# Kernel optimization log

Hardware: AMD Instinct MI355X
Metric: run time of the kernel (lower is better)

Reference implementation:

```python
import jax, jax.numpy as jnp
import numpy as np

B = 65536   # batch (agent-timesteps)
NN = 16     # neighbors per agent
NO = 32     # obstacles per agent
SD = 4      # state_dim_per_agent
D_ROBOT = 0.3
D_OBST = 0.5
B_GAMMA = 0.01
B_EXPH = 1.0
A_MIN, A_MAX = -2.0, 2.0
PHI_MIN, PHI_MAX = -2.0, 2.0


def _mlp2(h, W1, b1, W2, b2):
    # DeepSet sub-network: activation between layers, linear last (matches
    # 'for layer in layers[:-1]: x = act(layer(x)); x = layers[-1](x)')
    return jax.nn.relu(h @ W1 + b1) @ W2 + b2


def setup_inputs() -> dict:
    key = jax.random.key(0)
    ks = jax.random.split(key, 24)
    own = jax.random.normal(ks[0], (B, SD), dtype=jnp.float32)
    # relative positions with |component| in [0.5, 2.0] so norms exceed D_* (barrier well-defined)
    npos = jax.random.uniform(ks[1], (B, NN, 2), minval=0.5, maxval=2.0) * jnp.sign(jax.random.normal(ks[2], (B, NN, 2)))
    nvel = 0.1 * jax.random.normal(ks[3], (B, NN, 2))
    neigh = jnp.concatenate([npos, nvel], axis=-1).reshape(B, 4 * NN)
    opos = (jax.random.uniform(ks[4], (B, NO, 2), minval=0.5, maxval=2.0) * jnp.sign(jax.random.normal(ks[5], (B, NO, 2)))).reshape(B, 2 * NO)
    x = jnp.concatenate([jnp.full((B, 1), float(NN), dtype=jnp.float32), own, neigh, opos], axis=1)
    noise = 0.05 * jax.random.normal(ks[6], (B, 2), dtype=jnp.float32)  # the 0.05*N(0,1) action noise, made deterministic

    def lin(k, i, o):
        return 0.1 * jax.random.normal(k, (i, o), dtype=jnp.float32)

    return {
        'x': x, 'noise': noise,
        # neighbor DeepSet: phi 4->64->16, rho 16->64->8
        'pnW1': lin(ks[7], 4, 64),  'pnb1': jnp.zeros((64,), jnp.float32),
        'pnW2': lin(ks[8], 64, 16), 'pnb2': jnp.zeros((16,), jnp.float32),
        'rnW1': lin(ks[9], 16, 64), 'rnb1': jnp.zeros((64,), jnp.float32),
        'rnW2': lin(ks[10], 64, 8), 'rnb2': jnp.zeros((8,), jnp.float32),
        # obstacle DeepSet: phi 2->64->16, rho 16->64->8
        'poW1': lin(ks[11], 2, 64),  'pob1': jnp.zeros((64,), jnp.float32),
        'poW2': lin(ks[12], 64, 16), 'pob2': jnp.zeros((16,), jnp.float32),
        'roW1': lin(ks[13], 16, 64), 'rob1': jnp.zeros((64,), jnp.float32),
        'roW2': lin(ks[14], 64, 8),  'rob2': jnp.zeros((8,), jnp.float32),
        # psi: 18 -> 64 -> 64 -> 2
        'psW1': lin(ks[15], 18, 64), 'psb1': jnp.zeros((64,), jnp.float32),
        'psW2': lin(ks[16], 64, 64), 'psb2': jnp.zeros((64,), jnp.float32),
        'psW3': lin(ks[17], 64, 2),  'psb3': jnp.zeros((2,), jnp.float32),
    }


def reference(x, noise,
              pnW1, pnb1, pnW2, pnb2, rnW1, rnb1, rnW2, rnb2,
              poW1, pob1, poW2, pob2, roW1, rob1, roW2, rob2,
              psW1, psb1, psW2, psb2, psW3, psb3):
    b = x.shape[0]
    neigh = x[:, 5:5 + 4 * NN].reshape(b, NN, 4)   # per-neighbor relative state
    obst = x[:, 5 + 4 * NN:].reshape(b, NO, 2)      # per-obstacle relative pos

    # 'empty' (learned) action: DeepSets + psi MLP
    rho_n = _mlp2(_mlp2(neigh, pnW1, pnb1, pnW2, pnb2).sum(axis=1), rnW1, rnb1, rnW2, rnb2)
    rho_o = _mlp2(_mlp2(obst, poW1, pob1, poW2, pob2).sum(axis=1), roW1, rob1, roW2, rob2)
    g = x[:, 1:3]
    h = jnp.concatenate([rho_n, rho_o, g], axis=1)
    h = jax.nn.relu(h @ psW1 + psb1)
    h = jax.nn.relu(h @ psW2 + psb2)
    h = jnp.tanh(h @ psW3 + psb3)
    empty = (h + 1.0) / 2.0 * (PHI_MAX - PHI_MIN) + PHI_MIN

    # barrier terms, vectorized over all neighbors/obstacles at once:
    # A = b_gamma * P * ||P||^-1 * (||P|| - D)^(-b_exph), summed over edges
    def barrier_sum(P, D):
        nrm = jnp.linalg.norm(P, axis=-1, keepdims=True)   # [b, E, 1]
        H = nrm - D
        return (B_GAMMA * P / (nrm * H ** B_EXPH)).sum(axis=1)

    bar = barrier_sum(-neigh[..., :2], D_ROBOT) + barrier_sum(-obst, D_OBST)

    a = jnp.tanh(empty + bar + noise)
    return (a + 1.0) / 2.0 * (A_MAX - A_MIN) + A_MIN
```

## Files before the change

kernel.cpp:

```cpp
#include <hip/hip_runtime.h>

#define NN 16
#define NO 32
#define XCOLS 133

typedef _Float16 h8v __attribute__((ext_vector_type(8)));
typedef float f4v __attribute__((ext_vector_type(4)));
typedef unsigned ui4 __attribute__((ext_vector_type(4)));
typedef float f4u __attribute__((ext_vector_type(4), aligned(4)));

static __device__ __forceinline__ f4v MFMA(h8v a, h8v b, f4v c) {
    return __builtin_amdgcn_mfma_f32_16x16x32_f16(a, b, c, 0, 0, 0);
}
static __device__ __forceinline__ unsigned pkbits(float a, float b) {
    return __builtin_bit_cast(unsigned, __builtin_amdgcn_cvt_pkrtz(a, b));
}

__global__ void prep_frags(
    const float* __restrict__ pnW1, const float* __restrict__ pnW2,
    const float* __restrict__ rnW1, const float* __restrict__ rnW2,
    const float* __restrict__ poW1, const float* __restrict__ poW2,
    const float* __restrict__ roW1, const float* __restrict__ roW2,
    const float* __restrict__ psW1, const float* __restrict__ psW2,
    const float* __restrict__ psW3, unsigned* __restrict__ ws)
{
    const float* Ws[11] = {pnW1,pnW2,rnW1,rnW2,poW1,poW2,roW1,roW2,psW1,psW2,psW3};
    const int Kr[11]   = {4,64,16,64,2,64,16,64,18,64,64};
    const int Nr[11]   = {64,16,64,8,64,16,64,8,64,64,2};
    const int nkc[11]  = {1,2,1,2,1,2,1,2,1,2,2};
    const int nnt[11]  = {4,1,4,1,4,1,4,1,4,4,1};
    const int base[11] = {0,1024,1536,2560,3072,4096,4608,5632,6144,7168,9216};

    const int gid = blockIdx.x * 256 + threadIdx.x;
    int start = 0;
    #pragma unroll
    for (int a2 = 0; a2 < 11; ++a2) {
        const int n = nkc[a2] * nnt[a2] * 256;
        if (gid >= start && gid < start + n) {
            const int i = gid - start;
            const float* Wm = Ws[a2];
            const int K = Kr[a2], N = Nr[a2], nt_n = nnt[a2];
            const int d = i & 3, lane = (i >> 2) & 63, t = i >> 8;
            const int nt = t % nt_n, kc = t / nt_n;
            const int k = kc * 32 + 8 * (lane >> 4) + 2 * d;
            const int col = nt * 16 + (lane & 15);
            const float v0 = (k     < K && col < N) ? Wm[(k    ) * N + col] : 0.f;
            const float v1 = (k + 1 < K && col < N) ? Wm[(k + 1) * N + col] : 0.f;
            ws[base[a2] + i] = pkbits(v0, v1);
        }
        start += n;
    }
}

__global__ __launch_bounds__(64, 8) void barrier_net_kernel(
    const float* __restrict__ x, const float* __restrict__ noise,
    const float* __restrict__ pnb1, const float* __restrict__ pnb2,
    const float* __restrict__ rnb1, const float* __restrict__ rnb2,
    const float* __restrict__ pob1, const float* __restrict__ pob2,
    const float* __restrict__ rob1, const float* __restrict__ rob2,
    const float* __restrict__ psb1, const float* __restrict__ psb2,
    const float* __restrict__ psb3,
    const unsigned* __restrict__ wsu, float* __restrict__ out)
{
    __shared__ _Float16 W[3136];

    const int l = threadIdx.x;
    const int r = l & 15;
    const int g = l >> 4;
    const int eb = blockIdx.x * 16;

    float* barf = (float*)(W + 3072);
    const h8v* FB = (const h8v*)wsu;

    {
        unsigned* z = (unsigned*)(W + 2048);
        #pragma unroll
        for (int i = 0; i < 8; ++i) z[l + 64 * i] = 0u;
    }

    const size_t xrow = (size_t)(eb + r) * XCOLS;

    {
        float bq0 = 0.f, bq1 = 0.f;
        const float* pxn = x + xrow + 5;
        #pragma unroll
        for (int jj = 0; jj < 4; ++jj) {
            const int j = 4 * g + jj;
            const float v0 = pxn[4*j], v1 = pxn[4*j + 1];
            const float nrm = sqrtf(v0*v0 + v1*v1);
            const float cc = 0.01f * __builtin_amdgcn_rcpf(nrm * (nrm - 0.3f));
            bq0 -= cc * v0; bq1 -= cc * v1;
        }
        const float* pxo = x + xrow + 69;
        #pragma unroll
        for (int jj = 0; jj < 8; ++jj) {
            const int j = 8 * g + jj;
            const float v0 = pxo[2*j], v1 = pxo[2*j + 1];
            const float nrm = sqrtf(v0*v0 + v1*v1);
            const float cc = 0.01f * __builtin_amdgcn_rcpf(nrm * (nrm - 0.5f));
            bq0 -= cc * v0; bq1 -= cc * v1;
        }
        bq0 += __shfl_xor(bq0, 16); bq0 += __shfl_xor(bq0, 32);
        bq1 += __shfl_xor(bq1, 16); bq1 += __shfl_xor(bq1, 32);
        if (g == 0) { barf[2*r] = bq0; barf[2*r + 1] = bq1; }
    }

    {
        const h8v B0 = FB[0*64 + l], B1 = FB[1*64 + l];
        const h8v B2 = FB[2*64 + l], B3 = FB[3*64 + l];
        const f4v c0 = {pnb1[r], pnb1[r], pnb1[r], pnb1[r]};
        const f4v c1 = {pnb1[16+r], pnb1[16+r], pnb1[16+r], pnb1[16+r]};
        const f4v c2 = {pnb1[32+r], pnb1[32+r], pnb1[32+r], pnb1[32+r]};
        const f4v c3 = {pnb1[48+r], pnb1[48+r], pnb1[48+r], pnb1[48+r]};
        f4v s0 = {0,0,0,0}, s1 = {0,0,0,0}, s2 = {0,0,0,0}, s3 = {0,0,0,0};
        const float* px = x + xrow + 5;
        #pragma unroll 4
        for (int j = 0; j < NN; ++j) {
            const f4u v = *(const f4u*)(px + 4*j);
            ui4 au = {pkbits(v[0], v[1]), pkbits(v[2], v[3]), 0u, 0u};
            const h8v a = __builtin_bit_cast(h8v, au);
            const f4v d0 = MFMA(a, B0, c0);
            const f4v d1 = MFMA(a, B1, c1);
            const f4v d2 = MFMA(a, B2, c2);
            const f4v d3 = MFMA(a, B3, c3);
            #pragma unroll
            for (int q = 0; q < 4; ++q) {
                s0[q] += fmaxf(d0[q], 0.f); s1[q] += fmaxf(d1[q], 0.f);
                s2[q] += fmaxf(d2[q], 0.f); s3[q] += fmaxf(d3[q], 0.f);
            }
        }
        #pragma unroll
        for (int q = 0; q < 4; ++q) {
            const int e = 4 * g + q;
            const int m = (e & 7) << 3;
            W[e*64 + (( 0 + r) ^ m)] = (_Float16)s0[q];
            W[e*64 + ((16 + r) ^ m)] = (_Float16)s1[q];
            W[e*64 + ((32 + r) ^ m)] = (_Float16)s2[q];
            W[e*64 + ((48 + r) ^ m)] = (_Float16)s3[q];
        }
    }

    {
        const h8v B0 = FB[768 + 0*64 + l], B1 = FB[768 + 1*64 + l];
        const h8v B2 = FB[768 + 2*64 + l], B3 = FB[768 + 3*64 + l];
        const f4v c0 = {pob1[r], pob1[r], pob1[r], pob1[r]};
        const f4v c1 = {pob1[16+r], pob1[16+r], pob1[16+r], pob1[16+r]};
        const f4v c2 = {pob1[32+r], pob1[32+r], pob1[32+r], pob1[32+r]};
        const f4v c3 = {pob1[48+r], pob1[48+r], pob1[48+r], pob1[48+r]};
        f4v s0 = {0,0,0,0}, s1 = {0,0,0,0}, s2 = {0,0,0,0}, s3 = {0,0,0,0};
        const float* px = x + xrow + 69;
        #pragma unroll 2
        for (int t = 0; t < 16; ++t) {
            const f4u v = *(const f4u*)(px + 4*t);
            ui4 au0 = {pkbits(v[0], v[1]), 0u, 0u, 0u};
            ui4 au1 = {pkbits(v[2], v[3]), 0u, 0u, 0u};
            const h8v a0 = __builtin_bit_cast(h8v, au0);
            const h8v a1 = __builtin_bit_cast(h8v, au1);
            const f4v d0 = MFMA(a0, B0, c0); const f4v e0 = MFMA(a1, B0, c0);
            const f4v d1 = MFMA(a0, B1, c1); const f4v e1 = MFMA(a1, B1, c1);
            const f4v d2 = MFMA(a0, B2, c2); const f4v e2 = MFMA(a1, B2, c2);
            const f4v d3 = MFMA(a0, B3, c3); const f4v e3 = MFMA(a1, B3, c3);
            #pragma unroll
            for (int q = 0; q < 4; ++q) {
                s0[q] += fmaxf(d0[q], 0.f) + fmaxf(e0[q], 0.f);
                s1[q] += fmaxf(d1[q], 0.f) + fmaxf(e1[q], 0.f);
                s2[q] += fmaxf(d2[q], 0.f) + fmaxf(e2[q], 0.f);
                s3[q] += fmaxf(d3[q], 0.f) + fmaxf(e3[q], 0.f);
            }
        }
        #pragma unroll
        for (int q = 0; q < 4; ++q) {
            const int e = 4 * g + q;
            const int m = (e & 7) << 3;
            W[1024 + e*64 + (( 0 + r) ^ m)] = (_Float16)s0[q];
            W[1024 + e*64 + ((16 + r) ^ m)] = (_Float16)s1[q];
            W[1024 + e*64 + ((32 + r) ^ m)] = (_Float16)s2[q];
            W[1024 + e*64 + ((48 + r) ^ m)] = (_Float16)s3[q];
        }
    }

    {
        h8v a0 = *(const h8v*)&W[r*64 + (( 0 + 8*g) ^ ((r&7)<<3))];
        h8v a1 = *(const h8v*)&W[r*64 + ((32 + 8*g) ^ ((r&7)<<3))];
        h8v b0 = FB[256 + 0*64 + l];
        h8v b1 = FB[256 + 1*64 + l];
        const float bb = 16.f * pnb2[r];
        f4v c = {bb, bb, bb, bb};
        f4v d = MFMA(a1, b1, MFMA(a0, b0, c));
        #pragma unroll
        for (int q = 0; q < 4; ++q) {
            const int row = 4 * g + q;
            W[2048 + row*32 + (r ^ ((row&3)<<3))] = (_Float16)d[q];
        }
    }
    {
        h8v a = *(const h8v*)&W[2048 + r*32 + ((8*g) ^ ((r&3)<<3))];
        #pragma unroll
        for (int nt = 0; nt < 4; ++nt) {
            h8v b = FB[384 + nt*64 + l];
            const float bb = rnb1[16*nt + r];
            f4v c = {bb, bb, bb, bb};
            f4v d = MFMA(a, b, c);
            #pragma unroll
            for (int q = 0; q < 4; ++q) {
                const int row = 4 * g + q;
                W[row*64 + ((16*nt + r) ^ ((row&7)<<3))] = (_Float16)fmaxf(d[q], 0.f);
            }
        }
    }
    {
        h8v a0 = *(const h8v*)&W[r*64 + (( 0 + 8*g) ^ ((r&7)<<3))];
        h8v a1 = *(const h8v*)&W[r*64 + ((32 + 8*g) ^ ((r&7)<<3))];
        h8v b0 = FB[640 + 0*64 + l];
        h8v b1 = FB[640 + 1*64 + l];
        const float bb = (r < 8) ? rnb2[r & 7] : 0.f;
        f4v c = {bb, bb, bb, bb};
        f4v d = MFMA(a1, b1, MFMA(a0, b0, c));
        if (r < 8) {
            #pragma unroll
            for (int q = 0; q < 4; ++q) {
                const int row = 4 * g + q;
                W[2560 + row*32 + (r ^ ((row&3)<<3))] = (_Float16)d[q];
            }
        }
    }
    {
        h8v a0 = *(const h8v*)&W[1024 + r*64 + (( 0 + 8*g) ^ ((r&7)<<3))];
        h8v a1 = *(const h8v*)&W[1024 + r*64 + ((32 + 8*g) ^ ((r&7)<<3))];
        h8v b0 = FB[1024 + 0*64 + l];
        h8v b1 = FB[1024 + 1*64 + l];
        const float bb = 32.f * pob2[r];
        f4v c = {bb, bb, bb, bb};
        f4v d = MFMA(a1, b1, MFMA(a0, b0, c));
        #pragma unroll
        for (int q = 0; q < 4; ++q) {
            const int row = 4 * g + q;
            W[2048 + row*32 + (r ^ ((row&3)<<3))] = (_Float16)d[q];
        }
    }
    {
        h8v a = *(const h8v*)&W[2048 + r*32 + ((8*g) ^ ((r&3)<<3))];
        #pragma unroll
        for (int nt = 0; nt < 4; ++nt) {
            h8v b = FB[1152 + nt*64 + l];
            const float bb = rob1[16*nt + r];
            f4v c = {bb, bb, bb, bb};
            f4v d = MFMA(a, b, c);
            #pragma unroll
            for (int q = 0; q < 4; ++q) {
                const int row = 4 * g + q;
                W[row*64 + ((16*nt + r) ^ ((row&7)<<3))] = (_Float16)fmaxf(d[q], 0.f);
            }
        }
    }
    {
        h8v a0 = *(const h8v*)&W[r*64 + (( 0 + 8*g) ^ ((r&7)<<3))];
        h8v a1 = *(const h8v*)&W[r*64 + ((32 + 8*g) ^ ((r&7)<<3))];
        h8v b0 = FB[1408 + 0*64 + l];
        h8v b1 = FB[1408 + 1*64 + l];
        const float bb = (r < 8) ? rob2[r & 7] : 0.f;
        f4v c = {bb, bb, bb, bb};
        f4v d = MFMA(a1, b1, MFMA(a0, b0, c));
        if (r < 8) {
            #pragma unroll
            for (int q = 0; q < 4; ++q) {
                const int row = 4 * g + q;
                W[2560 + row*32 + ((8 + r) ^ ((row&3)<<3))] = (_Float16)d[q];
            }
        }
    }
    if (g == 0) {
        const float gx = x[xrow + 1];
        const float gy = x[xrow + 2];
        W[2560 + r*32 + (16 ^ ((r&3)<<3))] = (_Float16)gx;
        W[2560 + r*32 + (17 ^ ((r&3)<<3))] = (_Float16)gy;
    }
    {
        h8v a = *(const h8v*)&W[2560 + r*32 + ((8*g) ^ ((r&3)<<3))];
        #pragma unroll
        for (int nt = 0; nt < 4; ++nt) {
            h8v b = FB[1536 + nt*64 + l];
            const float bb = psb1[16*nt + r];
            f4v c = {bb, bb, bb, bb};
            f4v d = MFMA(a, b, c);
            #pragma unroll
            for (int q = 0; q < 4; ++q) {
                const int row = 4 * g + q;
                W[1024 + row*64 + ((16*nt + r) ^ ((row&7)<<3))] = (_Float16)fmaxf(d[q], 0.f);
            }
        }
    }
    {
        h8v a0 = *(const h8v*)&W[1024 + r*64 + (( 0 + 8*g) ^ ((r&7)<<3))];
        h8v a1 = *(const h8v*)&W[1024 + r*64 + ((32 + 8*g) ^ ((r&7)<<3))];
        #pragma unroll
        for (int nt = 0; nt < 4; ++nt) {
            h8v b0 = FB[1792 + (0*4 + nt)*64 + l];
            h8v b1 = FB[1792 + (1*4 + nt)*64 + l];
            const float bb = psb2[16*nt + r];
            f4v c = {bb, bb, bb, bb};
            f4v d = MFMA(a1, b1, MFMA(a0, b0, c));
            #pragma unroll
            for (int q = 0; q < 4; ++q) {
                const int row = 4 * g + q;
                W[row*64 + ((16*nt + r) ^ ((row&7)<<3))] = (_Float16)fmaxf(d[q], 0.f);
            }
        }
    }
    f4v dOut;
    {
        h8v a0 = *(const h8v*)&W[r*64 + (( 0 + 8*g) ^ ((r&7)<<3))];
        h8v a1 = *(const h8v*)&W[r*64 + ((32 + 8*g) ^ ((r&7)<<3))];
        h8v b0 = FB[2304 + 0*64 + l];
        h8v b1 = FB[2304 + 1*64 + l];
        const float bb = (r < 2) ? psb3[r & 1] : 0.f;
        f4v c = {bb, bb, bb, bb};
        dOut = MFMA(a1, b1, MFMA(a0, b0, c));
    }
    if (r < 2) {
        #pragma unroll
        for (int q = 0; q < 4; ++q) {
            const int e = 4 * g + q;
            const float o = dOut[q];
            const float bar = barf[e*2 + r];
            const float nz = noise[2 * (size_t)(eb + e) + r];
            const float av = tanhf(2.f * tanhf(o) + bar + nz);
            out[2 * (size_t)(eb + e) + r] = 2.f * av;
        }
    }
}

extern "C" void kernel_launch(void* const* d_in, const int* in_sizes, int n_in,
                              void* d_out, int out_size, void* d_ws, size_t ws_size,
                              hipStream_t stream) {
    const float* x    = (const float*)d_in[0];
    const float* nz   = (const float*)d_in[1];
    const float* pnW1 = (const float*)d_in[2];
    const float* pnb1 = (const float*)d_in[3];
    const float* pnW2 = (const float*)d_in[4];
    const float* pnb2 = (const float*)d_in[5];
    const float* rnW1 = (const float*)d_in[6];
    const float* rnb1 = (const float*)d_in[7];
    const float* rnW2 = (const float*)d_in[8];
    const float* rnb2 = (const float*)d_in[9];
    const float* poW1 = (const float*)d_in[10];
    const float* pob1 = (const float*)d_in[11];
    const float* poW2 = (const float*)d_in[12];
    const float* pob2 = (const float*)d_in[13];
    const float* roW1 = (const float*)d_in[14];
    const float* rob1 = (const float*)d_in[15];
    const float* roW2 = (const float*)d_in[16];
    const float* rob2 = (const float*)d_in[17];
    const float* psW1 = (const float*)d_in[18];
    const float* psb1 = (const float*)d_in[19];
    const float* psW2 = (const float*)d_in[20];
    const float* psb2 = (const float*)d_in[21];
    const float* psW3 = (const float*)d_in[22];
    const float* psb3 = (const float*)d_in[23];

    unsigned* ws = (unsigned*)d_ws;
    hipLaunchKernelGGL(prep_frags, dim3(38), dim3(256), 0, stream,
        pnW1, pnW2, rnW1, rnW2, poW1, poW2, roW1, roW2, psW1, psW2, psW3, ws);

    const int b = in_sizes[0] / XCOLS;
    hipLaunchKernelGGL(barrier_net_kernel, dim3(b / 16), dim3(64), 0, stream,
        x, nz, pnb1, pnb2, rnb1, rnb2, pob1, pob2, rob1, rob2,
        psb1, psb2, psb3, ws, (float*)d_out);
}
```

Before: 45.44 us.

## Fuse neighbor and obstacle DeepSet stages and pack four waves per block

```diff
diff --git a/kernel.cpp b/kernel.cpp
--- a/kernel.cpp
+++ b/kernel.cpp
@@ -52,7 +52,7 @@
     }
 }
 
-__global__ __launch_bounds__(64, 8) void barrier_net_kernel(
+__global__ __launch_bounds__(256, 4) void barrier_net_kernel(
     const float* __restrict__ x, const float* __restrict__ noise,
     const float* __restrict__ pnb1, const float* __restrict__ pnb2,
     const float* __restrict__ rnb1, const float* __restrict__ rnb2,
@@ -62,23 +62,88 @@
     const float* __restrict__ psb3,
     const unsigned* __restrict__ wsu, float* __restrict__ out)
 {
-    __shared__ _Float16 W[3136];
-
-    const int l = threadIdx.x;
+    __shared__ _Float16 smem[4][3648];
+
+    const int tid = threadIdx.x;
+    const int l = tid & 63;
+    const int w = tid >> 6;
     const int r = l & 15;
     const int g = l >> 4;
-    const int eb = blockIdx.x * 16;
-
-    float* barf = (float*)(W + 3072);
+    const int eb = blockIdx.x * 64 + w * 16;
+
+    _Float16* W = &smem[w][0];
+    float* barf = (float*)(W + 3584);
     const h8v* FB = (const h8v*)wsu;
 
     {
         unsigned* z = (unsigned*)(W + 2048);
         #pragma unroll
-        for (int i = 0; i < 8; ++i) z[l + 64 * i] = 0u;
+        for (int i = 0; i < 12; ++i) z[l + 64 * i] = 0u;
     }
 
     const size_t xrow = (size_t)(eb + r) * XCOLS;
+    const int sw8 = (r & 7) << 3;
+    const int sw4 = (r & 3) << 3;
+
+    {
+        const h8v BN0 = FB[0*64 + l], BN1 = FB[1*64 + l];
+        const h8v BN2 = FB[2*64 + l], BN3 = FB[3*64 + l];
+        const h8v BO0 = FB[768 + 0*64 + l], BO1 = FB[768 + 1*64 + l];
+        const h8v BO2 = FB[768 + 2*64 + l], BO3 = FB[768 + 3*64 + l];
+        const f4v cN0 = {pnb1[r], pnb1[r], pnb1[r], pnb1[r]};
+        const f4v cN1 = {pnb1[16+r], pnb1[16+r], pnb1[16+r], pnb1[16+r]};
+        const f4v cN2 = {pnb1[32+r], pnb1[32+r], pnb1[32+r], pnb1[32+r]};
+        const f4v cN3 = {pnb1[48+r], pnb1[48+r], pnb1[48+r], pnb1[48+r]};
+        const f4v cO0 = {pob1[r], pob1[r], pob1[r], pob1[r]};
+        const f4v cO1 = {pob1[16+r], pob1[16+r], pob1[16+r], pob1[16+r]};
+        const f4v cO2 = {pob1[32+r], pob1[32+r], pob1[32+r], pob1[32+r]};
+        const f4v cO3 = {pob1[48+r], pob1[48+r], pob1[48+r], pob1[48+r]};
+        f4v sN0 = {0,0,0,0}, sN1 = {0,0,0,0}, sN2 = {0,0,0,0}, sN3 = {0,0,0,0};
+        f4v sO0 = {0,0,0,0}, sO1 = {0,0,0,0}, sO2 = {0,0,0,0}, sO3 = {0,0,0,0};
+        const float* pxn = x + xrow + 5;
+        const float* pxo = x + xrow + 69;
+        #pragma unroll 2
+        for (int t = 0; t < 16; ++t) {
+            const f4u vN = *(const f4u*)(pxn + 4*t);
+            const f4u vO = *(const f4u*)(pxo + 4*t);
+            ui4 auN = {pkbits(vN[0], vN[1]), pkbits(vN[2], vN[3]), 0u, 0u};
+            ui4 auO0 = {pkbits(vO[0], vO[1]), 0u, 0u, 0u};
+            ui4 auO1 = {pkbits(vO[2], vO[3]), 0u, 0u, 0u};
+            const h8v aN  = __builtin_bit_cast(h8v, auN);
+            const h8v aO0 = __builtin_bit_cast(h8v, auO0);
+            const h8v aO1 = __builtin_bit_cast(h8v, auO1);
+            const f4v dN0 = MFMA(aN, BN0, cN0);
+            const f4v dN1 = MFMA(aN, BN1, cN1);
+            const f4v dN2 = MFMA(aN, BN2, cN2);
+            const f4v dN3 = MFMA(aN, BN3, cN3);
+            const f4v dO0 = MFMA(aO0, BO0, cO0); const f4v eO0 = MFMA(aO1, BO0, cO0);
+            const f4v dO1 = MFMA(aO0, BO1, cO1); const f4v eO1 = MFMA(aO1, BO1, cO1);
+            const f4v dO2 = MFMA(aO0, BO2, cO2); const f4v eO2 = MFMA(aO1, BO2, cO2);
+            const f4v dO3 = MFMA(aO0, BO3, cO3); const f4v eO3 = MFMA(aO1, BO3, cO3);
+            #pragma unroll
+            for (int q = 0; q < 4; ++q) {
+                sN0[q] += fmaxf(dN0[q], 0.f); sN1[q] += fmaxf(dN1[q], 0.f);
+                sN2[q] += fmaxf(dN2[q], 0.f); sN3[q] += fmaxf(dN3[q], 0.f);
+                sO0[q] += fmaxf(dO0[q], 0.f) + fmaxf(eO0[q], 0.f);
+                sO1[q] += fmaxf(dO1[q], 0.f) + fmaxf(eO1[q], 0.f);
+                sO2[q] += fmaxf(dO2[q], 0.f) + fmaxf(eO2[q], 0.f);
+                sO3[q] += fmaxf(dO3[q], 0.f) + fmaxf(eO3[q], 0.f);
+            }
+        }
+        #pragma unroll
+        for (int q = 0; q < 4; ++q) {
+            const int e = 4 * g + q;
+            const int m = (e & 7) << 3;
+            W[e*64 + (( 0 + r) ^ m)] = (_Float16)sN0[q];
+            W[e*64 + ((16 + r) ^ m)] = (_Float16)sN1[q];
+            W[e*64 + ((32 + r) ^ m)] = (_Float16)sN2[q];
+            W[e*64 + ((48 + r) ^ m)] = (_Float16)sN3[q];
+            W[1024 + e*64 + (( 0 + r) ^ m)] = (_Float16)sO0[q];
+            W[1024 + e*64 + ((16 + r) ^ m)] = (_Float16)sO1[q];
+            W[1024 + e*64 + ((32 + r) ^ m)] = (_Float16)sO2[q];
+            W[1024 + e*64 + ((48 + r) ^ m)] = (_Float16)sO3[q];
+        }
+    }
 
     {
         float bq0 = 0.f, bq1 = 0.f;
@@ -106,177 +171,79 @@
     }
 
     {
-        const h8v B0 = FB[0*64 + l], B1 = FB[1*64 + l];
-        const h8v B2 = FB[2*64 + l], B3 = FB[3*64 + l];
-        const f4v c0 = {pnb1[r], pnb1[r], pnb1[r], pnb1[r]};
-        const f4v c1 = {pnb1[16+r], pnb1[16+r], pnb1[16+r], pnb1[16+r]};
-        const f4v c2 = {pnb1[32+r], pnb1[32+r], pnb1[32+r], pnb1[32+r]};
-        const f4v c3 = {pnb1[48+r], pnb1[48+r], pnb1[48+r], pnb1[48+r]};
-        f4v s0 = {0,0,0,0}, s1 = {0,0,0,0}, s2 = {0,0,0,0}, s3 = {0,0,0,0};
-        const float* px = x + xrow + 5;
-        #pragma unroll 4
-        for (int j = 0; j < NN; ++j) {
-            const f4u v = *(const f4u*)(px + 4*j);
-            ui4 au = {pkbits(v[0], v[1]), pkbits(v[2], v[3]), 0u, 0u};
-            const h8v a = __builtin_bit_cast(h8v, au);
-            const f4v d0 = MFMA(a, B0, c0);
-            const f4v d1 = MFMA(a, B1, c1);
-            const f4v d2 = MFMA(a, B2, c2);
-            const f4v d3 = MFMA(a, B3, c3);
-            #pragma unroll
-            for (int q = 0; q < 4; ++q) {
-                s0[q] += fmaxf(d0[q], 0.f); s1[q] += fmaxf(d1[q], 0.f);
-                s2[q] += fmaxf(d2[q], 0.f); s3[q] += fmaxf(d3[q], 0.f);
-            }
-        }
-        #pragma unroll
-        for (int q = 0; q < 4; ++q) {
-            const int e = 4 * g + q;
-            const int m = (e & 7) << 3;
-            W[e*64 + (( 0 + r) ^ m)] = (_Float16)s0[q];
-            W[e*64 + ((16 + r) ^ m)] = (_Float16)s1[q];
-            W[e*64 + ((32 + r) ^ m)] = (_Float16)s2[q];
-            W[e*64 + ((48 + r) ^ m)] = (_Float16)s3[q];
-        }
-    }
-
-    {
-        const h8v B0 = FB[768 + 0*64 + l], B1 = FB[768 + 1*64 + l];
-        const h8v B2 = FB[768 + 2*64 + l], B3 = FB[768 + 3*64 + l];
-        const f4v c0 = {pob1[r], pob1[r], pob1[r], pob1[r]};
-        const f4v c1 = {pob1[16+r], pob1[16+r], pob1[16+r], pob1[16+r]};
-        const f4v c2 = {pob1[32+r], pob1[32+r], pob1[32+r], pob1[32+r]};
-        const f4v c3 = {pob1[48+r], pob1[48+r], pob1[48+r], pob1[48+r]};
-        f4v s0 = {0,0,0,0}, s1 = {0,0,0,0}, s2 = {0,0,0,0}, s3 = {0,0,0,0};
-        const float* px = x + xrow + 69;
-        #pragma unroll 2
-        for (int t = 0; t < 16; ++t) {
-            const f4u v = *(const f4u*)(px + 4*t);
-            ui4 au0 = {pkbits(v[0], v[1]), 0u, 0u, 0u};
-            ui4 au1 = {pkbits(v[2], v[3]), 0u, 0u, 0u};
-            const h8v a0 = __builtin_bit_cast(h8v, au0);
-            const h8v a1 = __builtin_bit_cast(h8v, au1);
-            const f4v d0 = MFMA(a0, B0, c0); const f4v e0 = MFMA(a1, B0, c0);
-            const f4v d1 = MFMA(a0, B1, c1); const f4v e1 = MFMA(a1, B1, c1);
-            const f4v d2 = MFMA(a0, B2, c2); const f4v e2 = MFMA(a1, B2, c2);
-            const f4v d3 = MFMA(a0, B3, c3); const f4v e3 = MFMA(a1, B3, c3);
-            #pragma unroll
-            for (int q = 0; q < 4; ++q) {
-                s0[q] += fmaxf(d0[q], 0.f) + fmaxf(e0[q], 0.f);
-                s1[q] += fmaxf(d1[q], 0.f) + fmaxf(e1[q], 0.f);
-                s2[q] += fmaxf(d2[q], 0.f) + fmaxf(e2[q], 0.f);
-                s3[q] += fmaxf(d3[q], 0.f) + fmaxf(e3[q], 0.f);
-            }
-        }
-        #pragma unroll
-        for (int q = 0; q < 4; ++q) {
-            const int e = 4 * g + q;
-            const int m = (e & 7) << 3;
-            W[1024 + e*64 + (( 0 + r) ^ m)] = (_Float16)s0[q];
-            W[1024 + e*64 + ((16 + r) ^ m)] = (_Float16)s1[q];
-            W[1024 + e*64 + ((32 + r) ^ m)] = (_Float16)s2[q];
-            W[1024 + e*64 + ((48 + r) ^ m)] = (_Float16)s3[q];
-        }
-    }
-
-    {
-        h8v a0 = *(const h8v*)&W[r*64 + (( 0 + 8*g) ^ ((r&7)<<3))];
-        h8v a1 = *(const h8v*)&W[r*64 + ((32 + 8*g) ^ ((r&7)<<3))];
-        h8v b0 = FB[256 + 0*64 + l];
-        h8v b1 = FB[256 + 1*64 + l];
-        const float bb = 16.f * pnb2[r];
-        f4v c = {bb, bb, bb, bb};
-        f4v d = MFMA(a1, b1, MFMA(a0, b0, c));
+        h8v aN0 = *(const h8v*)&W[r*64 + (( 0 + 8*g) ^ sw8)];
+        h8v aN1 = *(const h8v*)&W[r*64 + ((32 + 8*g) ^ sw8)];
+        h8v aO0 = *(const h8v*)&W[1024 + r*64 + (( 0 + 8*g) ^ sw8)];
+        h8v aO1 = *(const h8v*)&W[1024 + r*64 + ((32 + 8*g) ^ sw8)];
+        h8v bN0 = FB[256 + 0*64 + l], bN1 = FB[256 + 1*64 + l];
+        h8v bO0 = FB[1024 + 0*64 + l], bO1 = FB[1024 + 1*64 + l];
+        const float bbN = 16.f * pnb2[r];
+        const float bbO = 32.f * pob2[r];
+        f4v cN = {bbN, bbN, bbN, bbN};
+        f4v cO = {bbO, bbO, bbO, bbO};
+        f4v dN = MFMA(aN1, bN1, MFMA(aN0, bN0, cN));
+        f4v dO = MFMA(aO1, bO1, MFMA(aO0, bO0, cO));
         #pragma unroll
         for (int q = 0; q < 4; ++q) {
             const int row = 4 * g + q;
-            W[2048 + row*32 + (r ^ ((row&3)<<3))] = (_Float16)d[q];
-        }
-    }
-    {
-        h8v a = *(const h8v*)&W[2048 + r*32 + ((8*g) ^ ((r&3)<<3))];
+            const int sm = (row & 3) << 3;
+            W[2048 + row*32 + (r ^ sm)] = (_Float16)dN[q];
+            W[2560 + row*32 + (r ^ sm)] = (_Float16)dO[q];
+        }
+    }
+    {
+        h8v aN = *(const h8v*)&W[2048 + r*32 + ((8*g) ^ sw4)];
+        h8v aO = *(const h8v*)&W[2560 + r*32 + ((8*g) ^ sw4)];
         #pragma unroll
         for (int nt = 0; nt < 4; ++nt) {
-            h8v b = FB[384 + nt*64 + l];
-            const float bb = rnb1[16*nt + r];
-            f4v c = {bb, bb, bb, bb};
-            f4v d = MFMA(a, b, c);
+            h8v bN = FB[384 + nt*64 + l];
+            h8v bO = FB[1152 + nt*64 + l];
+            const float bbN = rnb1[16*nt + r];
+            const float bbO = rob1[16*nt + r];
+            f4v cN = {bbN, bbN, bbN, bbN};
+            f4v cO = {bbO, bbO, bbO, bbO};
+            f4v dN = MFMA(aN, bN, cN);
+            f4v dO = MFMA(aO, bO, cO);
             #pragma unroll
             for (int q = 0; q < 4; ++q) {
                 const int row = 4 * g + q;
-                W[row*64 + ((16*nt + r) ^ ((row&7)<<3))] = (_Float16)fmaxf(d[q], 0.f);
-            }
-        }
-    }
-    {
-        h8v a0 = *(const h8v*)&W[r*64 + (( 0 + 8*g) ^ ((r&7)<<3))];
-        h8v a1 = *(const h8v*)&W[r*64 + ((32 + 8*g) ^ ((r&7)<<3))];
-        h8v b0 = FB[640 + 0*64 + l];
-        h8v b1 = FB[640 + 1*64 + l];
-        const float bb = (r < 8) ? rnb2[r & 7] : 0.f;
-        f4v c = {bb, bb, bb, bb};
-        f4v d = MFMA(a1, b1, MFMA(a0, b0, c));
+                const int sm = (row & 7) << 3;
+                W[row*64 + ((16*nt + r) ^ sm)] = (_Float16)fmaxf(dN[q], 0.f);
+                W[1024 + row*64 + ((16*nt + r) ^ sm)] = (_Float16)fmaxf(dO[q], 0.f);
+            }
+        }
+    }
+    {
+        h8v aN0 = *(const h8v*)&W[r*64 + (( 0 + 8*g) ^ sw8)];
+        h8v aN1 = *(const h8v*)&W[r*64 + ((32 + 8*g) ^ sw8)];
+        h8v aO0 = *(const h8v*)&W[1024 + r*64 + (( 0 + 8*g) ^ sw8)];
+        h8v aO1 = *(const h8v*)&W[1024 + r*64 + ((32 + 8*g) ^ sw8)];
+        h8v bN0 = FB[640 + 0*64 + l], bN1 = FB[640 + 1*64 + l];
+        h8v bO0 = FB[1408 + 0*64 + l], bO1 = FB[1408 + 1*64 + l];
+        const float bbN = (r < 8) ? rnb2[r & 7] : 0.f;
+        const float bbO = (r < 8) ? rob2[r & 7] : 0.f;
+        f4v cN = {bbN, bbN, bbN, bbN};
+        f4v cO = {bbO, bbO, bbO, bbO};
+        f4v dN = MFMA(aN1, bN1, MFMA(aN0, bN0, cN));
+        f4v dO = MFMA(aO1, bO1, MFMA(aO0, bO0, cO));
         if (r < 8) {
             #pragma unroll
             for (int q = 0; q < 4; ++q) {
                 const int row = 4 * g + q;
-                W[2560 + row*32 + (r ^ ((row&3)<<3))] = (_Float16)d[q];
-            }
-        }
-    }
-    {
-        h8v a0 = *(const h8v*)&W[1024 + r*64 + (( 0 + 8*g) ^ ((r&7)<<3))];
-        h8v a1 = *(const h8v*)&W[1024 + r*64 + ((32 + 8*g) ^ ((r&7)<<3))];
-        h8v b0 = FB[1024 + 0*64 + l];
-        h8v b1 = FB[1024 + 1*64 + l];
-        const float bb = 32.f * pob2[r];
-        f4v c = {bb, bb, bb, bb};
-        f4v d = MFMA(a1, b1, MFMA(a0, b0, c));
-        #pragma unroll
-        for (int q = 0; q < 4; ++q) {
-            const int row = 4 * g + q;
-            W[2048 + row*32 + (r ^ ((row&3)<<3))] = (_Float16)d[q];
-        }
-    }
-    {
-        h8v a = *(const h8v*)&W[2048 + r*32 + ((8*g) ^ ((r&3)<<3))];
-        #pragma unroll
-        for (int nt = 0; nt < 4; ++nt) {
-            h8v b = FB[1152 + nt*64 + l];
-            const float bb = rob1[16*nt + r];
-            f4v c = {bb, bb, bb, bb};
-            f4v d = MFMA(a, b, c);
-            #pragma unroll
-            for (int q = 0; q < 4; ++q) {
-                const int row = 4 * g + q;
-                W[row*64 + ((16*nt + r) ^ ((row&7)<<3))] = (_Float16)fmaxf(d[q], 0.f);
-            }
-        }
-    }
-    {
-        h8v a0 = *(const h8v*)&W[r*64 + (( 0 + 8*g) ^ ((r&7)<<3))];
-        h8v a1 = *(const h8v*)&W[r*64 + ((32 + 8*g) ^ ((r&7)<<3))];
-        h8v b0 = FB[1408 + 0*64 + l];
-        h8v b1 = FB[1408 + 1*64 + l];
-        const float bb = (r < 8) ? rob2[r & 7] : 0.f;
-        f4v c = {bb, bb, bb, bb};
-        f4v d = MFMA(a1, b1, MFMA(a0, b0, c));
-        if (r < 8) {
-            #pragma unroll
-            for (int q = 0; q < 4; ++q) {
-                const int row = 4 * g + q;
-                W[2560 + row*32 + ((8 + r) ^ ((row&3)<<3))] = (_Float16)d[q];
+                const int sm = (row & 3) << 3;
+                W[3072 + row*32 + (r ^ sm)] = (_Float16)dN[q];
+                W[3072 + row*32 + ((8 + r) ^ sm)] = (_Float16)dO[q];
             }
         }
     }
     if (g == 0) {
         const float gx = x[xrow + 1];
         const float gy = x[xrow + 2];
-        W[2560 + r*32 + (16 ^ ((r&3)<<3))] = (_Float16)gx;
-        W[2560 + r*32 + (17 ^ ((r&3)<<3))] = (_Float16)gy;
-    }
-    {
-        h8v a = *(const h8v*)&W[2560 + r*32 + ((8*g) ^ ((r&3)<<3))];
+        W[3072 + r*32 + (16 ^ sw4)] = (_Float16)gx;
+        W[3072 + r*32 + (17 ^ sw4)] = (_Float16)gy;
+    }
+    {
+        h8v a = *(const h8v*)&W[3072 + r*32 + ((8*g) ^ sw4)];
         #pragma unroll
         for (int nt = 0; nt < 4; ++nt) {
             h8v b = FB[1536 + nt*64 + l];
@@ -286,13 +253,13 @@
             #pragma unroll
             for (int q = 0; q < 4; ++q) {
                 const int row = 4 * g + q;
-                W[1024 + row*64 + ((16*nt + r) ^ ((row&7)<<3))] = (_Float16)fmaxf(d[q], 0.f);
-            }
-        }
-    }
-    {
-        h8v a0 = *(const h8v*)&W[1024 + r*64 + (( 0 + 8*g) ^ ((r&7)<<3))];
-        h8v a1 = *(const h8v*)&W[1024 + r*64 + ((32 + 8*g) ^ ((r&7)<<3))];
+                W[1024 + row*64 + ((16*nt + r) ^ ((row & 7) << 3))] = (_Float16)fmaxf(d[q], 0.f);
+            }
+        }
+    }
+    {
+        h8v a0 = *(const h8v*)&W[1024 + r*64 + (( 0 + 8*g) ^ sw8)];
+        h8v a1 = *(const h8v*)&W[1024 + r*64 + ((32 + 8*g) ^ sw8)];
         #pragma unroll
         for (int nt = 0; nt < 4; ++nt) {
             h8v b0 = FB[1792 + (0*4 + nt)*64 + l];
@@ -303,14 +270,14 @@
             #pragma unroll
             for (int q = 0; q < 4; ++q) {
                 const int row = 4 * g + q;
-                W[row*64 + ((16*nt + r) ^ ((row&7)<<3))] = (_Float16)fmaxf(d[q], 0.f);
+                W[row*64 + ((16*nt + r) ^ ((row & 7) << 3))] = (_Float16)fmaxf(d[q], 0.f);
             }
         }
     }
     f4v dOut;
     {
-        h8v a0 = *(const h8v*)&W[r*64 + (( 0 + 8*g) ^ ((r&7)<<3))];
-        h8v a1 = *(const h8v*)&W[r*64 + ((32 + 8*g) ^ ((r&7)<<3))];
+        h8v a0 = *(const h8v*)&W[r*64 + (( 0 + 8*g) ^ sw8)];
+        h8v a1 = *(const h8v*)&W[r*64 + ((32 + 8*g) ^ sw8)];
         h8v b0 = FB[2304 + 0*64 + l];
         h8v b1 = FB[2304 + 1*64 + l];
         const float bb = (r < 2) ? psb3[r & 1] : 0.f;
@@ -363,7 +330,7 @@
         pnW1, pnW2, rnW1, rnW2, poW1, poW2, roW1, roW2, psW1, psW2, psW3, ws);
 
     const int b = in_sizes[0] / XCOLS;
-    hipLaunchKernelGGL(barrier_net_kernel, dim3(b / 16), dim3(64), 0, stream,
+    hipLaunchKernelGGL(barrier_net_kernel, dim3(b / 64), dim3(256), 0, stream,
         x, nz, pnb1, pnb2, rnb1, rnb2, pob1, pob2, rob1, rob2,
         psb1, psb2, psb3, ws, (float*)d_out);
 }
```

Result: slower. 170.2 us (+274.6%).

## Stage input rows in shared memory as packed fp16 with coalesced loads

Applied to the files above, without the earlier changes.

```diff
diff --git a/kernel.cpp b/kernel.cpp
--- a/kernel.cpp
+++ b/kernel.cpp
@@ -5,9 +5,10 @@
 #define XCOLS 133
 
 typedef _Float16 h8v __attribute__((ext_vector_type(8)));
+typedef _Float16 h2 __attribute__((ext_vector_type(2)));
 typedef float f4v __attribute__((ext_vector_type(4)));
 typedef unsigned ui4 __attribute__((ext_vector_type(4)));
-typedef float f4u __attribute__((ext_vector_type(4), aligned(4)));
+typedef float f2u __attribute__((ext_vector_type(2), aligned(4)));
 
 static __device__ __forceinline__ f4v MFMA(h8v a, h8v b, f4v c) {
     return __builtin_amdgcn_mfma_f32_16x16x32_f16(a, b, c, 0, 0, 0);
@@ -15,6 +16,7 @@
 static __device__ __forceinline__ unsigned pkbits(float a, float b) {
     return __builtin_bit_cast(unsigned, __builtin_amdgcn_cvt_pkrtz(a, b));
 }
+static __device__ __forceinline__ h2 u2h(unsigned v) { return __builtin_bit_cast(h2, v); }
 
 __global__ void prep_frags(
     const float* __restrict__ pnW1, const float* __restrict__ pnW2,
@@ -52,7 +54,7 @@
     }
 }
 
-__global__ __launch_bounds__(64, 8) void barrier_net_kernel(
+__global__ __launch_bounds__(64, 4) void barrier_net_kernel(
     const float* __restrict__ x, const float* __restrict__ noise,
     const float* __restrict__ pnb1, const float* __restrict__ pnb2,
     const float* __restrict__ rnb1, const float* __restrict__ rnb2,
@@ -62,6 +64,7 @@
     const float* __restrict__ psb3,
     const unsigned* __restrict__ wsu, float* __restrict__ out)
 {
+    __shared__ unsigned XS[16 * 66];
     __shared__ _Float16 W[3136];
 
     const int l = threadIdx.x;
@@ -73,29 +76,43 @@
     const h8v* FB = (const h8v*)wsu;
 
     {
+        const float* base = x + (size_t)eb * XCOLS;
+        f2u raw[16];
+        #pragma unroll
+        for (int it = 0; it < 16; ++it)
+            raw[it] = *(const f2u*)(base + (size_t)it * XCOLS + 5 + 2 * l);
+        f2u graw = {0.f, 0.f};
+        if (l < 16) graw = *(const f2u*)(base + (size_t)l * XCOLS + 1);
+        #pragma unroll
+        for (int it = 0; it < 16; ++it)
+            XS[it * 66 + l] = pkbits(raw[it][0], raw[it][1]);
+        if (l < 16) XS[l * 66 + 64] = pkbits(graw[0], graw[1]);
+    }
+
+    {
         unsigned* z = (unsigned*)(W + 2048);
         #pragma unroll
         for (int i = 0; i < 8; ++i) z[l + 64 * i] = 0u;
     }
 
-    const size_t xrow = (size_t)(eb + r) * XCOLS;
+    const int rowb = r * 66;
+    const int sw8 = (r & 7) << 3;
+    const int sw4 = (r & 3) << 3;
 
     {
         float bq0 = 0.f, bq1 = 0.f;
-        const float* pxn = x + xrow + 5;
         #pragma unroll
         for (int jj = 0; jj < 4; ++jj) {
-            const int j = 4 * g + jj;
-            const float v0 = pxn[4*j], v1 = pxn[4*j + 1];
+            const h2 v = u2h(XS[rowb + 2 * (4 * g + jj)]);
+            const float v0 = (float)v[0], v1 = (float)v[1];
             const float nrm = sqrtf(v0*v0 + v1*v1);
             const float cc = 0.01f * __builtin_amdgcn_rcpf(nrm * (nrm - 0.3f));
             bq0 -= cc * v0; bq1 -= cc * v1;
         }
-        const float* pxo = x + xrow + 69;
         #pragma unroll
         for (int jj = 0; jj < 8; ++jj) {
-            const int j = 8 * g + jj;
-            const float v0 = pxo[2*j], v1 = pxo[2*j + 1];
+            const h2 v = u2h(XS[rowb + 32 + 8 * g + jj]);
+            const float v0 = (float)v[0], v1 = (float)v[1];
             const float nrm = sqrtf(v0*v0 + v1*v1);
             const float cc = 0.01f * __builtin_amdgcn_rcpf(nrm * (nrm - 0.5f));
             bq0 -= cc * v0; bq1 -= cc * v1;
@@ -113,11 +130,10 @@
         const f4v c2 = {pnb1[32+r], pnb1[32+r], pnb1[32+r], pnb1[32+r]};
         const f4v c3 = {pnb1[48+r], pnb1[48+r], pnb1[48+r], pnb1[48+r]};
         f4v s0 = {0,0,0,0}, s1 = {0,0,0,0}, s2 = {0,0,0,0}, s3 = {0,0,0,0};
-        const float* px = x + xrow + 5;
         #pragma unroll 4
         for (int j = 0; j < NN; ++j) {
-            const f4u v = *(const f4u*)(px + 4*j);
-            ui4 au = {pkbits(v[0], v[1]), pkbits(v[2], v[3]), 0u, 0u};
+            const uint2 np = *(const uint2*)&XS[rowb + 2 * j];
+            ui4 au = {np.x, np.y, 0u, 0u};
             const h8v a = __builtin_bit_cast(h8v, au);
             const f4v d0 = MFMA(a, B0, c0);
             const f4v d1 = MFMA(a, B1, c1);
@@ -148,12 +164,11 @@
         const f4v c2 = {pob1[32+r], pob1[32+r], pob1[32+r], pob1[32+r]};
         const f4v c3 = {pob1[48+r], pob1[48+r], pob1[48+r], pob1[48+r]};
         f4v s0 = {0,0,0,0}, s1 = {0,0,0,0}, s2 = {0,0,0,0}, s3 = {0,0,0,0};
-        const float* px = x + xrow + 69;
         #pragma unroll 2
         for (int t = 0; t < 16; ++t) {
-            const f4u v = *(const f4u*)(px + 4*t);
-            ui4 au0 = {pkbits(v[0], v[1]), 0u, 0u, 0u};
-            ui4 au1 = {pkbits(v[2], v[3]), 0u, 0u, 0u};
+            const uint2 op = *(const uint2*)&XS[rowb + 32 + 2 * t];
+            ui4 au0 = {op.x, 0u, 0u, 0u};
+            ui4 au1 = {op.y, 0u, 0u, 0u};
             const h8v a0 = __builtin_bit_cast(h8v, au0);
             const h8v a1 = __builtin_bit_cast(h8v, au1);
             const f4v d0 = MFMA(a0, B0, c0); const f4v e0 = MFMA(a1, B0, c0);
@@ -180,8 +195,8 @@
     }
 
     {
-        h8v a0 = *(const h8v*)&W[r*64 + (( 0 + 8*g) ^ ((r&7)<<3))];
-        h8v a1 = *(const h8v*)&W[r*64 + ((32 + 8*g) ^ ((r&7)<<3))];
+        h8v a0 = *(const h8v*)&W[r*64 + (( 0 + 8*g) ^ sw8)];
+        h8v a1 = *(const h8v*)&W[r*64 + ((32 + 8*g) ^ sw8)];
         h8v b0 = FB[256 + 0*64 + l];
         h8v b1 = FB[256 + 1*64 + l];
         const float bb = 16.f * pnb2[r];
@@ -194,7 +209,7 @@
         }
     }
     {
-        h8v a = *(const h8v*)&W[2048 + r*32 + ((8*g) ^ ((r&3)<<3))];
+        h8v a = *(const h8v*)&W[2048 + r*32 + ((8*g) ^ sw4)];
         #pragma unroll
         for (int nt = 0; nt < 4; ++nt) {
             h8v b = FB[384 + nt*64 + l];
@@ -209,8 +224,8 @@
         }
     }
     {
-        h8v a0 = *(const h8v*)&W[r*64 + (( 0 + 8*g) ^ ((r&7)<<3))];
-        h8v a1 = *(const h8v*)&W[r*64 + ((32 + 8*g) ^ ((r&7)<<3))];
+        h8v a0 = *(const h8v*)&W[r*64 + (( 0 + 8*g) ^ sw8)];
+        h8v a1 = *(const h8v*)&W[r*64 + ((32 + 8*g) ^ sw8)];
         h8v b0 = FB[640 + 0*64 + l];
         h8v b1 = FB[640 + 1*64 + l];
         const float bb = (r < 8) ? rnb2[r & 7] : 0.f;
@@ -225,8 +240,8 @@
         }
     }
     {
-        h8v a0 = *(const h8v*)&W[1024 + r*64 + (( 0 + 8*g) ^ ((r&7)<<3))];
-        h8v a1 = *(const h8v*)&W[1024 + r*64 + ((32 + 8*g) ^ ((r&7)<<3))];
+        h8v a0 = *(const h8v*)&W[1024 + r*64 + (( 0 + 8*g) ^ sw8)];
+        h8v a1 = *(const h8v*)&W[1024 + r*64 + ((32 + 8*g) ^ sw8)];
         h8v b0 = FB[1024 + 0*64 + l];
         h8v b1 = FB[1024 + 1*64 + l];
         const float bb = 32.f * pob2[r];
@@ -239,7 +254,7 @@
         }
     }
     {
-        h8v a = *(const h8v*)&W[2048 + r*32 + ((8*g) ^ ((r&3)<<3))];
+        h8v a = *(const h8v*)&W[2048 + r*32 + ((8*g) ^ sw4)];
         #pragma unroll
         for (int nt = 0; nt < 4; ++nt) {
             h8v b = FB[1152 + nt*64 + l];
@@ -254,8 +269,8 @@
         }
     }
     {
-        h8v a0 = *(const h8v*)&W[r*64 + (( 0 + 8*g) ^ ((r&7)<<3))];
-        h8v a1 = *(const h8v*)&W[r*64 + ((32 + 8*g) ^ ((r&7)<<3))];
+        h8v a0 = *(const h8v*)&W[r*64 + (( 0 + 8*g) ^ sw8)];
+        h8v a1 = *(const h8v*)&W[r*64 + ((32 + 8*g) ^ sw8)];
         h8v b0 = FB[1408 + 0*64 + l];
         h8v b1 = FB[1408 + 1*64 + l];
         const float bb = (r < 8) ? rob2[r & 7] : 0.f;
@@ -270,13 +285,12 @@
         }
     }
     if (g == 0) {
-        const float gx = x[xrow + 1];
-        const float gy = x[xrow + 2];
-        W[2560 + r*32 + (16 ^ ((r&3)<<3))] = (_Float16)gx;
-        W[2560 + r*32 + (17 ^ ((r&3)<<3))] = (_Float16)gy;
-    }
-    {
-        h8v a = *(const h8v*)&W[2560 + r*32 + ((8*g) ^ ((r&3)<<3))];
+        const h2 gv = u2h(XS[rowb + 64]);
+        W[2560 + r*32 + (16 ^ sw4)] = gv[0];
+        W[2560 + r*32 + (17 ^ sw4)] = gv[1];
+    }
+    {
+        h8v a = *(const h8v*)&W[2560 + r*32 + ((8*g) ^ sw4)];
         #pragma unroll
         for (int nt = 0; nt < 4; ++nt) {
             h8v b = FB[1536 + nt*64 + l];
@@ -291,8 +305,8 @@
         }
     }
     {
-        h8v a0 = *(const h8v*)&W[1024 + r*64 + (( 0 + 8*g) ^ ((r&7)<<3))];
-        h8v a1 = *(const h8v*)&W[1024 + r*64 + ((32 + 8*g) ^ ((r&7)<<3))];
+        h8v a0 = *(const h8v*)&W[1024 + r*64 + (( 0 + 8*g) ^ sw8)];
+        h8v a1 = *(const h8v*)&W[1024 + r*64 + ((32 + 8*g) ^ sw8)];
         #pragma unroll
         for (int nt = 0; nt < 4; ++nt) {
             h8v b0 = FB[1792 + (0*4 + nt)*64 + l];
@@ -309,8 +323,8 @@
     }
     f4v dOut;
     {
-        h8v a0 = *(const h8v*)&W[r*64 + (( 0 + 8*g) ^ ((r&7)<<3))];
-        h8v a1 = *(const h8v*)&W[r*64 + ((32 + 8*g) ^ ((r&7)<<3))];
+        h8v a0 = *(const h8v*)&W[r*64 + (( 0 + 8*g) ^ sw8)];
+        h8v a1 = *(const h8v*)&W[r*64 + ((32 + 8*g) ^ sw8)];
         h8v b0 = FB[2304 + 0*64 + l];
         h8v b1 = FB[2304 + 1*64 + l];
         const float bb = (r < 2) ? psb3[r & 1] : 0.f;
```

Result: no change. 44.68 us, median of 2 (-1.7%).
